# Kernel optimization log

Measured on AMD Instinct MI355X. Metric: run time of the kernel, lower is better.

Reference implementation:

```python
import jax, jax.numpy as jnp
import numpy as np
import math

EMBED_DIM = 1024
NUM_HEADS = 16
NUM_KV_HEADS = 16
DEPTH = 12
HEAD_DIM = EMBED_DIM // NUM_HEADS // 2  # 32
LAMBDA_INIT = 0.8 - 0.6 * math.exp(-0.3 * DEPTH)
EPS = 1e-5
THETA = 0.0001


def rope(q):
    # q: (b, s, h, d) with interleaved pairs, matches apply_rotary_pos_emb
    b, s, h, d = q.shape
    pos = jnp.arange(s, dtype=jnp.float32)[:, None]                      # (s,1)
    freq = 1.0 / (THETA ** (2.0 * jnp.arange(d // 2, dtype=jnp.float32) / d))
    ang = pos * freq                                                     # (s, d/2)
    cos = jnp.cos(ang)[None, :, None, :].astype(q.dtype)
    sin = jnp.sin(ang)[None, :, None, :].astype(q.dtype)
    qr = q.reshape(b, s, h, d // 2, 2)
    q0, q1 = qr[..., 0], qr[..., 1]
    out = jnp.stack([q0 * cos - q1 * sin, q0 * sin + q1 * cos], axis=-1)
    return out.reshape(q.shape)


def setup_inputs() -> dict:
    key = jax.random.key(0)
    ks = jax.random.split(key, 10)
    d = EMBED_DIM
    sd = 1.0 / math.sqrt(d)
    return {
        "x": jax.random.normal(ks[0], (1, 2048, d), dtype=jnp.float32),
        "Wq": jax.random.normal(ks[1], (d, d), dtype=jnp.float32) * sd,
        "Wk": jax.random.normal(ks[2], (d, d), dtype=jnp.float32) * sd,
        "Wv": jax.random.normal(ks[3], (d, d), dtype=jnp.float32) * sd,
        "Wo": jax.random.normal(ks[4], (d, d), dtype=jnp.float32) * sd,
        "lambda_q1": jax.random.normal(ks[5], (HEAD_DIM,), dtype=jnp.float32) * 0.1,
        "lambda_k1": jax.random.normal(ks[6], (HEAD_DIM,), dtype=jnp.float32) * 0.1,
        "lambda_q2": jax.random.normal(ks[7], (HEAD_DIM,), dtype=jnp.float32) * 0.1,
        "lambda_k2": jax.random.normal(ks[8], (HEAD_DIM,), dtype=jnp.float32) * 0.1,
        "subln_g": jnp.ones((2 * HEAD_DIM,), dtype=jnp.float32),
    }


def reference(x, Wq, Wk, Wv, Wo, lambda_q1, lambda_k1, lambda_q2, lambda_k2, subln_g):
    b, s, d = x.shape
    H, hd = NUM_HEADS, HEAD_DIM
    scaling = hd ** (-0.5)

    q = (x @ Wq).reshape(b, s, 2 * H, hd)
    k = (x @ Wk).reshape(b, s, 2 * NUM_KV_HEADS, hd)
    v = (x @ Wv).reshape(b, s, NUM_KV_HEADS, 2 * hd)

    q = rope(q).transpose(0, 2, 1, 3) * scaling   # (b, 2H, s, hd)
    k = rope(k).transpose(0, 2, 1, 3)             # (b, 2H, s, hd)  (n_rep = 1)
    v = v.transpose(0, 2, 1, 3)                   # (b, H, s, 2hd)

    scores = jnp.einsum("bhqd,bhkd->bhqk", q, k)  # (b, 2H, s, s)
    probs = jax.nn.softmax(scores.astype(jnp.float32), axis=-1).astype(scores.dtype)

    lam1 = jnp.exp(jnp.sum(lambda_q1 * lambda_k1))
    lam2 = jnp.exp(jnp.sum(lambda_q2 * lambda_k2))
    lam = (lam1 - lam2 + LAMBDA_INIT).astype(q.dtype)

    probs = probs.reshape(b, H, 2, s, s)
    w = probs[:, :, 0] - lam * probs[:, :, 1]     # (b, H, s, s)

    attn = jnp.einsum("bhqk,bhkd->bhqd", w, v)    # (b, H, s, 2hd)
    rms = jax.lax.rsqrt(jnp.mean(attn * attn, axis=-1, keepdims=True) + EPS)
    attn = attn * rms * subln_g
    attn = attn * (1.0 - LAMBDA_INIT)

    attn = attn.transpose(0, 2, 1, 3).reshape(b, s, H * 2 * hd)
    return attn @ Wo
```

## Files before the change

kernel.cpp:

```cpp
#include <hip/hip_runtime.h>
#include <math.h>

#define S 2048
#define D 1024
#define NH 16
#define HD 32
#define HD2 64

static constexpr float SCALE_Q_EXP2  = 0.17677669529663687f * 1.4426950408889634f;
static constexpr float LAMBDA_INIT_F = 0.78360576653162450f;
static constexpr float ONE_MINUS_LI  = 0.21639423346837553f;

typedef unsigned short u16;
typedef unsigned int   u32;
typedef __attribute__((ext_vector_type(4)))  unsigned short u16x4;
typedef __attribute__((ext_vector_type(8)))  short          bfrag;
typedef __attribute__((ext_vector_type(16))) float          f16acc;
typedef __attribute__((ext_vector_type(4)))  unsigned int   uint4v;

__device__ __forceinline__ u16 f2bf(float f) {
    u32 u = __builtin_bit_cast(u32, f);
    return (u16)((u + 0x7FFFu + ((u >> 16) & 1u)) >> 16);
}
__device__ __forceinline__ f16acc fillv(float v) {
    f16acc z;
#pragma unroll
    for (int i = 0; i < 16; ++i) z[i] = v;
    return z;
}
__device__ __forceinline__ float exp2_raw(float x) {
#if __has_builtin(__builtin_amdgcn_exp2f)
    return __builtin_amdgcn_exp2f(x);
#else
    float r;
    asm volatile("v_exp_f32 %0, %1\n\ts_nop 1" : "=v"(r) : "v"(x));
    return r;
#endif
}
#define MFMA(a, b, c) __builtin_amdgcn_mfma_f32_32x32x16_bf16(a, b, c, 0, 0, 0)

__device__ __forceinline__ void gload16(const u16* src, u16* lds) {
    __builtin_amdgcn_global_load_lds((const __attribute__((address_space(1))) void*)src,
                                     (__attribute__((address_space(3))) void*)lds, 16, 0, 0);
}

__global__ void prep_kernel(const float* __restrict__ lq1, const float* __restrict__ lk1,
                            const float* __restrict__ lq2, const float* __restrict__ lk2,
                            float* __restrict__ cosT, float* __restrict__ sinT,
                            float* __restrict__ lamOut) {
    int idx = blockIdx.x * blockDim.x + threadIdx.x;
    if (idx < S * 16) {
        int p = idx >> 4;
        int m = idx & 15;
        const double base = (double)1.0e-4f;
        float pf   = (float)pow(base, (double)m * (1.0 / 16.0));
        float freq = 1.0f / pf;
        float angf = (float)p * freq;
        double a = (double)angf;
        cosT[idx] = (float)cos(a);
        sinT[idx] = (float)sin(a);
    }
    if (blockIdx.x == 0 && threadIdx.x == 0) {
        float s1 = 0.f, s2 = 0.f;
        for (int i = 0; i < HD; ++i) {
            s1 += lq1[i] * lk1[i];
            s2 += lq2[i] * lk2[i];
        }
        *lamOut = expf(s1) - expf(s2) + LAMBDA_INIT_F;
    }
}

__global__ __launch_bounds__(256)
void convert_kernel(const float* __restrict__ x,  const float* __restrict__ Wq,
                    const float* __restrict__ Wk, const float* __restrict__ Wv,
                    const float* __restrict__ Wo,
                    u16* __restrict__ xb,  u16* __restrict__ WqT, u16* __restrict__ WkT,
                    u16* __restrict__ WvT, u16* __restrict__ WoT) {
    const int z = blockIdx.y;
    if (z == 0) {
        const int i = blockIdx.x * 256 + threadIdx.x;
        const float4 v = *(const float4*)&x[(size_t)i * 4];
        u16x4 r; r.x = f2bf(v.x); r.y = f2bf(v.y); r.z = f2bf(v.z); r.w = f2bf(v.w);
        *(u16x4*)&xb[(size_t)i * 4] = r;
        return;
    }
    const int b = blockIdx.x;
    if (b >= 256) return;
    __shared__ u16 Ts[64][66];
    const float* W = (z == 1) ? Wq : (z == 2) ? Wk : (z == 3) ? Wv : Wo;
    u16* T = (z == 1) ? WqT : (z == 2) ? WkT : (z == 3) ? WvT : WoT;
    const int k0 = (b >> 4) * 64, n0 = (b & 15) * 64;
    const int rg = threadIdx.x >> 4, cc = (threadIdx.x & 15) * 4;
#pragma unroll
    for (int i = 0; i < 4; ++i) {
        const int r = rg * 4 + i;
        const float4 v = *(const float4*)&W[(size_t)(k0 + r) * D + n0 + cc];
        Ts[r][cc + 0] = f2bf(v.x); Ts[r][cc + 1] = f2bf(v.y);
        Ts[r][cc + 2] = f2bf(v.z); Ts[r][cc + 3] = f2bf(v.w);
    }
    __syncthreads();
#pragma unroll
    for (int i = 0; i < 4; ++i) {
        const int rn = rg * 4 + i;
        u16x4 res;
        res.x = Ts[cc + 0][rn]; res.y = Ts[cc + 1][rn];
        res.z = Ts[cc + 2][rn]; res.w = Ts[cc + 3][rn];
        *(u16x4*)&T[(size_t)(n0 + rn) * D + k0 + cc] = res;
    }
}

template<int MODE>
__global__ __launch_bounds__(256)
void mm_kernel(const u16* __restrict__ Ab, const u16* __restrict__ B0,
               const u16* __restrict__ B1, const u16* __restrict__ B2,
               const float* __restrict__ cosT, const float* __restrict__ sinT,
               u16* __restrict__ Qb, u16* __restrict__ Kb2, u16* __restrict__ VT,
               float* __restrict__ Of) {
    __shared__ u16 As[128 * 32];
    __shared__ u16 Bs[128 * 32];

    const int nb   = blockIdx.x;
    const int row0 = blockIdx.y * 128;
    const int tid  = threadIdx.x;
    const int wave = tid >> 6;
    const int lane = tid & 63;
    const int ql   = lane & 31;
    const int hi   = lane >> 5;
    const int wr   = wave >> 1;
    const int wc   = wave & 1;

    const u16* Bt;
    int col0B;
    if (MODE == 0) {
        Bt = (nb < 8) ? B0 : (nb < 16) ? B1 : B2;
        col0B = (nb & 7) * 128;
    } else {
        Bt = B0;
        col0B = nb * 128;
    }

    const int rIn  = lane >> 2;
    const int kof  = 8 * (lane & 3);
    const size_t aRow0 = (size_t)(row0 + 16 * wave       + rIn) * D + kof;
    const size_t aRow1 = (size_t)(row0 + 16 * (wave + 4) + rIn) * D + kof;
    const size_t bRow0 = (size_t)(col0B + 16 * wave       + rIn) * D + kof;
    const size_t bRow1 = (size_t)(col0B + 16 * (wave + 4) + rIn) * D + kof;
    u16* ldsA0 = &As[512 * wave + 8 * lane];
    u16* ldsA1 = &As[512 * (wave + 4) + 8 * lane];
    u16* ldsB0 = &Bs[512 * wave + 8 * lane];
    u16* ldsB1 = &Bs[512 * (wave + 4) + 8 * lane];

    const int aoff = (wr * 64 + ql) * 32 + hi * 8;
    const int boff = (wc * 64 + ql) * 32 + hi * 8;

    f16acc acc00 = fillv(0.f), acc01 = fillv(0.f), acc10 = fillv(0.f), acc11 = fillv(0.f);

    for (int kk = 0; kk < D; kk += 32) {
        gload16(Ab + aRow0 + kk, ldsA0);
        gload16(Ab + aRow1 + kk, ldsA1);
        gload16(Bt + bRow0 + kk, ldsB0);
        gload16(Bt + bRow1 + kk, ldsB1);
        __syncthreads();
#pragma unroll
        for (int ks = 0; ks < 2; ++ks) {
            const bfrag a0 = *(const bfrag*)&As[aoff + ks * 16];
            const bfrag a1 = *(const bfrag*)&As[aoff + 32 * 32 + ks * 16];
            const bfrag b0 = *(const bfrag*)&Bs[boff + ks * 16];
            const bfrag b1 = *(const bfrag*)&Bs[boff + 32 * 32 + ks * 16];
            acc00 = MFMA(a0, b0, acc00);
            acc01 = MFMA(a0, b1, acc01);
            acc10 = MFMA(a1, b0, acc10);
            acc11 = MFMA(a1, b1, acc11);
        }
        __syncthreads();
    }

    f16acc accA[2][2];
    accA[0][0] = acc00; accA[0][1] = acc01; accA[1][0] = acc10; accA[1][1] = acc11;

    if (MODE == 0 && nb < 8) {
        const int m = ql >> 1;
        const bool ev = (ql & 1) == 0;
#pragma unroll
        for (int i = 0; i < 2; ++i)
#pragma unroll
        for (int j = 0; j < 2; ++j) {
            const int n = (nb & 7) * 128 + wc * 64 + j * 32 + ql;
            const int head = n >> 5;
            u16* hb = Qb + (size_t)head * S * HD;
#pragma unroll
            for (int r = 0; r < 16; ++r) {
                const int row = row0 + wr * 64 + i * 32 + 4 * hi + (r & 3) + 8 * (r >> 2);
                const float self = accA[i][j][r];
                const float part = __shfl_xor(self, 1);
                const float c = cosT[(row << 4) + m], s = sinT[(row << 4) + m];
                const float res = ev ? (self * c - part * s) : (part * s + self * c);
                hb[(size_t)row * HD + ql] = f2bf(res * SCALE_Q_EXP2);
            }
        }
    } else if (MODE == 0 && nb < 16) {
        const int m = ql >> 1;
        const bool ev = (ql & 1) == 0;
#pragma unroll
        for (int i = 0; i < 2; ++i)
#pragma unroll
        for (int j = 0; j < 2; ++j) {
            const int n = (nb & 7) * 128 + wc * 64 + j * 32 + ql;
            const int h2 = n >> 5;
            const int d  = n & 31;
            const int dpl = (d >> 3) * 256 + (d & 7);
            u16* hb = Kb2 + (size_t)h2 * 65536;
#pragma unroll
            for (int r = 0; r < 16; ++r) {
                const int row = row0 + wr * 64 + i * 32 + 4 * hi + (r & 3) + 8 * (r >> 2);
                const float self = accA[i][j][r];
                const float part = __shfl_xor(self, 1);
                const float c = cosT[(row << 4) + m], s = sinT[(row << 4) + m];
                const float res = ev ? (self * c - part * s) : (part * s + self * c);
                hb[(row >> 5) * 1024 + dpl + (row & 31) * 8] = f2bf(res);
            }
        }
    } else if (MODE == 0) {
#pragma unroll
        for (int i = 0; i < 2; ++i)
#pragma unroll
        for (int j = 0; j < 2; ++j) {
            const int n = (nb & 7) * 128 + wc * 64 + j * 32 + ql;
            const int head = n >> 6, d = n & 63;
            const int dt = d >> 5, dl = d & 31;
            u16* tb = VT + (size_t)head * 131072;
#pragma unroll
            for (int q = 0; q < 4; ++q) {
                const int row = row0 + wr * 64 + i * 32 + 4 * hi + 8 * q;
                const int idx = (row >> 5) * 2048 + (dt * 4 + q) * 256 + dl * 8 + 4 * hi;
                u16x4 res;
                res.x = f2bf(accA[i][j][4 * q + 0]);
                res.y = f2bf(accA[i][j][4 * q + 1]);
                res.z = f2bf(accA[i][j][4 * q + 2]);
                res.w = f2bf(accA[i][j][4 * q + 3]);
                *(u16x4*)&tb[idx] = res;
            }
        }
    } else {
#pragma unroll
        for (int i = 0; i < 2; ++i)
#pragma unroll
        for (int j = 0; j < 2; ++j) {
            const int gcol = col0B + wc * 64 + j * 32 + ql;
#pragma unroll
            for (int r = 0; r < 16; ++r) {
                const int row = row0 + wr * 64 + i * 32 + 4 * hi + (r & 3) + 8 * (r >> 2);
                Of[(size_t)row * D + gcol] = accA[i][j][r];
            }
        }
    }
}

__global__ __launch_bounds__(512, 2)
void attn_mfma(const u16* __restrict__ Qb, const u16* __restrict__ Kb2,
               const u16* __restrict__ Vt2, const float* __restrict__ lamPtr,
               const float* __restrict__ g, u16* __restrict__ AO) {
    const int bid  = blockIdx.x;
    const int h    = (bid & 7) * 2 + ((bid >> 3) >> 5);
    const int bx   = (bid >> 3) & 31;
    const int tid  = threadIdx.x;
    const int wave = tid >> 6;
    const int lane = tid & 63;
    const int hi   = lane >> 5;
    const int ql   = lane & 31;
    const int t    = wave >> 2;
    const int wv   = wave & 3;
    const int q0   = (bx * 2 + t) * 32;
    const int cbase = wv * 16;

    __shared__ float CMB[2][64][66];

    const u16* qp1 = Qb + ((size_t)(2 * h) * S + q0 + ql) * HD + 8 * hi;
    const u16* qp2 = qp1 + (size_t)S * HD;
    bfrag qf1[2], qf2[2];
    qf1[0] = *(const bfrag*)(qp1);      qf1[1] = *(const bfrag*)(qp1 + 16);
    qf2[0] = *(const bfrag*)(qp2);      qf2[1] = *(const bfrag*)(qp2 + 16);

    const u16* k1g = Kb2 + (size_t)(2 * h) * 65536;
    const u16* k2g = k1g + 65536;
    const u16* vg  = Vt2 + (size_t)h * 131072;
    const int kro  = ql * 8;

    const f16acc ZR = fillv(0.f);
    uint4v ou; ou[0] = ou[1] = ou[2] = ou[3] = 0x3F803F80u;
    const bfrag ONES = __builtin_bit_cast(bfrag, ou);

    f16acc acc1[2], acc2[2];
    acc1[0] = fillv(0.f); acc1[1] = fillv(0.f);
    acc2[0] = fillv(0.f); acc2[1] = fillv(0.f);
    float l1 = 0.f, l2 = 0.f;

    bfrag kA1[2], kA2[2], kB1[2], kB2[2];
    bfrag vA[2][2], vB[2][2];
#pragma unroll
    for (int s = 0; s < 2; ++s) {
        kA1[s] = *(const bfrag*)(k1g + (size_t)cbase * 1024 + (2 * s + hi) * 256 + kro);
        kA2[s] = *(const bfrag*)(k2g + (size_t)cbase * 1024 + (2 * s + hi) * 256 + kro);
#pragma unroll
        for (int dt = 0; dt < 2; ++dt)
            vA[s][dt] = *(const bfrag*)(vg + (size_t)cbase * 2048 + (dt * 4 + 2 * s + hi) * 256 + kro);
    }

    auto body = [&](bfrag (&kc1)[2], bfrag (&kc2)[2], bfrag (&vc)[2][2],
                    bfrag (&kn1)[2], bfrag (&kn2)[2], bfrag (&vn)[2][2], int cn) {
        const u16* k1c = k1g + (size_t)cn * 1024;
        const u16* k2c = k2g + (size_t)cn * 1024;
        const u16* vvc = vg + (size_t)cn * 2048;
#pragma unroll
        for (int s = 0; s < 2; ++s) {
            kn1[s] = *(const bfrag*)(k1c + (2 * s + hi) * 256 + kro);
            kn2[s] = *(const bfrag*)(k2c + (2 * s + hi) * 256 + kro);
#pragma unroll
            for (int dt = 0; dt < 2; ++dt)
                vn[s][dt] = *(const bfrag*)(vvc + (dt * 4 + 2 * s + hi) * 256 + kro);
        }

        __builtin_amdgcn_s_setprio(1);
        f16acc s1 = MFMA(kc1[0], qf1[0], ZR);  s1 = MFMA(kc1[1], qf1[1], s1);
        f16acc s2 = MFMA(kc2[0], qf2[0], ZR);  s2 = MFMA(kc2[1], qf2[1], s2);
        __builtin_amdgcn_s_setprio(0);

#pragma unroll
        for (int r = 0; r < 16; ++r) {
            s1[r] = exp2_raw(s1[r]);
            s2[r] = exp2_raw(s2[r]);
        }

        u32 w1[8], w2[8];
#pragma unroll
        for (int j = 0; j < 8; ++j) {
            asm("v_cvt_pk_bf16_f32 %0, %1, %2" : "=v"(w1[j]) : "v"(s1[2 * j]), "v"(s1[2 * j + 1]));
            asm("v_cvt_pk_bf16_f32 %0, %1, %2" : "=v"(w2[j]) : "v"(s2[2 * j]), "v"(s2[2 * j + 1]));
        }
        asm("v_permlane32_swap_b32 %0, %1" : "+v"(w1[0]), "+v"(w1[2]));
        asm("v_permlane32_swap_b32 %0, %1" : "+v"(w1[1]), "+v"(w1[3]));
        asm("v_permlane32_swap_b32 %0, %1" : "+v"(w1[4]), "+v"(w1[6]));
        asm("v_permlane32_swap_b32 %0, %1" : "+v"(w1[5]), "+v"(w1[7]));
        asm("v_permlane32_swap_b32 %0, %1" : "+v"(w2[0]), "+v"(w2[2]));
        asm("v_permlane32_swap_b32 %0, %1" : "+v"(w2[1]), "+v"(w2[3]));
        asm("v_permlane32_swap_b32 %0, %1" : "+v"(w2[4]), "+v"(w2[6]));
        asm("v_permlane32_swap_b32 %0, %1" : "+v"(w2[5]), "+v"(w2[7]));
        uint4v u;
        bfrag p1[2], p2[2];
        u[0] = w1[0]; u[1] = w1[1]; u[2] = w1[2]; u[3] = w1[3];
        p1[0] = __builtin_bit_cast(bfrag, u);
        u[0] = w1[4]; u[1] = w1[5]; u[2] = w1[6]; u[3] = w1[7];
        p1[1] = __builtin_bit_cast(bfrag, u);
        u[0] = w2[0]; u[1] = w2[1]; u[2] = w2[2]; u[3] = w2[3];
        p2[0] = __builtin_bit_cast(bfrag, u);
        u[0] = w2[4]; u[1] = w2[5]; u[2] = w2[6]; u[3] = w2[7];
        p2[1] = __builtin_bit_cast(bfrag, u);

        __builtin_amdgcn_s_setprio(1);
        acc1[0] = MFMA(vc[0][0], p1[0], acc1[0]);
        acc1[0] = MFMA(vc[1][0], p1[1], acc1[0]);
        acc1[1] = MFMA(vc[0][1], p1[0], acc1[1]);
        acc1[1] = MFMA(vc[1][1], p1[1], acc1[1]);
        acc2[0] = MFMA(vc[0][0], p2[0], acc2[0]);
        acc2[0] = MFMA(vc[1][0], p2[1], acc2[0]);
        acc2[1] = MFMA(vc[0][1], p2[0], acc2[1]);
        acc2[1] = MFMA(vc[1][1], p2[1], acc2[1]);
        f16acc t1 = MFMA(ONES, p1[0], ZR);  t1 = MFMA(ONES, p1[1], t1);
        f16acc t2 = MFMA(ONES, p2[0], ZR);  t2 = MFMA(ONES, p2[1], t2);
        __builtin_amdgcn_s_setprio(0);
        l1 += t1[0];
        l2 += t2[0];
    };

    for (int i = 0; i < 16; i += 2) {
        const int c0 = cbase + i;
        body(kA1, kA2, vA, kB1, kB2, vB, c0 + 1);
        const int c2 = (i + 2 < 16) ? c0 + 2 : c0 + 1;
        body(kB1, kB2, vB, kA1, kA2, vA, c2);
    }

#pragma unroll 1
    for (int p = 1; p < 4; ++p) {
        if (wv == p) {
            float* c0 = &CMB[t][lane][0];
#pragma unroll
            for (int dt = 0; dt < 2; ++dt)
#pragma unroll
                for (int r = 0; r < 16; ++r) {
                    c0[dt * 16 + r]      = acc1[dt][r];
                    c0[32 + dt * 16 + r] = acc2[dt][r];
                }
            c0[64] = l1; c0[65] = l2;
        }
        __syncthreads();
        if (wv == 0) {
            const float* c0 = &CMB[t][lane][0];
#pragma unroll
            for (int dt = 0; dt < 2; ++dt)
#pragma unroll
                for (int r = 0; r < 16; ++r) {
                    acc1[dt][r] += c0[dt * 16 + r];
                    acc2[dt][r] += c0[32 + dt * 16 + r];
                }
            l1 += c0[64]; l2 += c0[65];
        }
        __syncthreads();
    }

    if (wv == 0) {
        const float lam = *lamPtr;
        const float inv1 = 1.0f / l1, inv2 = 1.0f / l2;
        float o_[2][16];
        float ss = 0.f;
#pragma unroll
        for (int dt = 0; dt < 2; ++dt)
#pragma unroll
            for (int r = 0; r < 16; ++r) {
                float o = acc1[dt][r] * inv1 - lam * (acc2[dt][r] * inv2);
                o_[dt][r] = o;
                ss += o * o;
            }
        ss += __shfl_xor(ss, 32);
        const float rs = rsqrtf(ss * (1.0f / 64.0f) + 1e-5f);

        u16* aorow = AO + (size_t)(q0 + ql) * D + h * 64;
#pragma unroll
        for (int dt = 0; dt < 2; ++dt)
#pragma unroll
            for (int G = 0; G < 4; ++G) {
                const int dbase = dt * 32 + G * 8 + hi * 4;
                const float4 gv = *(const float4*)&g[dbase];
                u16x4 res;
                res.x = f2bf(o_[dt][4 * G + 0] * rs * gv.x * ONE_MINUS_LI);
                res.y = f2bf(o_[dt][4 * G + 1] * rs * gv.y * ONE_MINUS_LI);
                res.z = f2bf(o_[dt][4 * G + 2] * rs * gv.z * ONE_MINUS_LI);
                res.w = f2bf(o_[dt][4 * G + 3] * rs * gv.w * ONE_MINUS_LI);
                *(u16x4*)&aorow[dbase] = res;
            }
    }
}

extern "C" void kernel_launch(void* const* d_in, const int* in_sizes, int n_in,
                              void* d_out, int out_size, void* d_ws, size_t ws_size,
                              hipStream_t stream) {
    const float* x   = (const float*)d_in[0];
    const float* Wq  = (const float*)d_in[1];
    const float* Wk  = (const float*)d_in[2];
    const float* Wv  = (const float*)d_in[3];
    const float* Wo  = (const float*)d_in[4];
    const float* lq1 = (const float*)d_in[5];
    const float* lk1 = (const float*)d_in[6];
    const float* lq2 = (const float*)d_in[7];
    const float* lk2 = (const float*)d_in[8];
    const float* g   = (const float*)d_in[9];
    float* out = (float*)d_out;

    char* ws = (char*)d_ws;
    float* cosT = (float*)(ws);
    float* sinT = (float*)(ws + 131072);
    float* lam  = (float*)(ws + 262144);
    char*  b    = ws + 262400;
    u16*   Qb   = (u16*)(b);
    u16*   Kb2  = (u16*)(b + 4194304);
    u16*   VT   = (u16*)(b + 8388608);
    u16*   AO   = (u16*)(b + 12582912);
    u16*   xb   = (u16*)(b + 16777216);
    u16*   WqT  = (u16*)(b + 20971520);
    u16*   WkT  = (u16*)(b + 23068672);
    u16*   WvT  = (u16*)(b + 25165824);
    u16*   WoT  = (u16*)(b + 27262976);

    prep_kernel<<<128, 256, 0, stream>>>(lq1, lk1, lq2, lk2, cosT, sinT, lam);
    convert_kernel<<<dim3(2048, 5), 256, 0, stream>>>(x, Wq, Wk, Wv, Wo,
                                                      xb, WqT, WkT, WvT, WoT);

    mm_kernel<0><<<dim3(24, 16), 256, 0, stream>>>(xb, WqT, WkT, WvT, cosT, sinT,
                                                   Qb, Kb2, VT, nullptr);

    attn_mfma<<<512, 512, 0, stream>>>(Qb, Kb2, VT, lam, g, AO);

    mm_kernel<1><<<dim3(8, 16), 256, 0, stream>>>(AO, WoT, nullptr, nullptr, cosT, sinT,
                                                  nullptr, nullptr, nullptr, out);
}
```

Baseline: 107.7 us.

## Software-pipeline attention loop so PV MFMA of previous chunk overlaps softmax

New measurement: 114.3 us. 6.2% more time.

```diff
diff --git a/kernel.cpp b/kernel.cpp
--- a/kernel.cpp
+++ b/kernel.cpp
@@ -295,42 +295,33 @@
     acc2[0] = fillv(0.f); acc2[1] = fillv(0.f);
     float l1 = 0.f, l2 = 0.f;
 
-    bfrag kA1[2], kA2[2], kB1[2], kB2[2];
-    bfrag vA[2][2], vB[2][2];
-#pragma unroll
-    for (int s = 0; s < 2; ++s) {
-        kA1[s] = *(const bfrag*)(k1g + (size_t)cbase * 1024 + (2 * s + hi) * 256 + kro);
-        kA2[s] = *(const bfrag*)(k2g + (size_t)cbase * 1024 + (2 * s + hi) * 256 + kro);
-#pragma unroll
-        for (int dt = 0; dt < 2; ++dt)
-            vA[s][dt] = *(const bfrag*)(vg + (size_t)cbase * 2048 + (dt * 4 + 2 * s + hi) * 256 + kro);
-    }
-
-    auto body = [&](bfrag (&kc1)[2], bfrag (&kc2)[2], bfrag (&vc)[2][2],
-                    bfrag (&kn1)[2], bfrag (&kn2)[2], bfrag (&vn)[2][2], int cn) {
-        const u16* k1c = k1g + (size_t)cn * 1024;
-        const u16* k2c = k2g + (size_t)cn * 1024;
-        const u16* vvc = vg + (size_t)cn * 2048;
+    bfrag K1s[2][2], K2s[2][2];
+    bfrag Vs[3][2][2];
+    bfrag pC1[2], pC2[2];
+
+    auto loadK = [&](int set, int c) {
+        const u16* k1c = k1g + (size_t)c * 1024;
+        const u16* k2c = k2g + (size_t)c * 1024;
 #pragma unroll
         for (int s = 0; s < 2; ++s) {
-            kn1[s] = *(const bfrag*)(k1c + (2 * s + hi) * 256 + kro);
-            kn2[s] = *(const bfrag*)(k2c + (2 * s + hi) * 256 + kro);
+            K1s[set][s] = *(const bfrag*)(k1c + (2 * s + hi) * 256 + kro);
+            K2s[set][s] = *(const bfrag*)(k2c + (2 * s + hi) * 256 + kro);
+        }
+    };
+    auto loadV = [&](int set, int c) {
+        const u16* vvc = vg + (size_t)c * 2048;
+#pragma unroll
+        for (int s = 0; s < 2; ++s)
 #pragma unroll
             for (int dt = 0; dt < 2; ++dt)
-                vn[s][dt] = *(const bfrag*)(vvc + (dt * 4 + 2 * s + hi) * 256 + kro);
-        }
-
-        __builtin_amdgcn_s_setprio(1);
-        f16acc s1 = MFMA(kc1[0], qf1[0], ZR);  s1 = MFMA(kc1[1], qf1[1], s1);
-        f16acc s2 = MFMA(kc2[0], qf2[0], ZR);  s2 = MFMA(kc2[1], qf2[1], s2);
-        __builtin_amdgcn_s_setprio(0);
-
+                Vs[set][s][dt] = *(const bfrag*)(vvc + (dt * 4 + 2 * s + hi) * 256 + kro);
+    };
+    auto doSM = [&](f16acc& s1, f16acc& s2) {
 #pragma unroll
         for (int r = 0; r < 16; ++r) {
             s1[r] = exp2_raw(s1[r]);
             s2[r] = exp2_raw(s2[r]);
         }
-
         u32 w1[8], w2[8];
 #pragma unroll
         for (int j = 0; j < 8; ++j) {
@@ -346,38 +337,60 @@
         asm("v_permlane32_swap_b32 %0, %1" : "+v"(w2[4]), "+v"(w2[6]));
         asm("v_permlane32_swap_b32 %0, %1" : "+v"(w2[5]), "+v"(w2[7]));
         uint4v u;
-        bfrag p1[2], p2[2];
         u[0] = w1[0]; u[1] = w1[1]; u[2] = w1[2]; u[3] = w1[3];
-        p1[0] = __builtin_bit_cast(bfrag, u);
+        pC1[0] = __builtin_bit_cast(bfrag, u);
         u[0] = w1[4]; u[1] = w1[5]; u[2] = w1[6]; u[3] = w1[7];
-        p1[1] = __builtin_bit_cast(bfrag, u);
+        pC1[1] = __builtin_bit_cast(bfrag, u);
         u[0] = w2[0]; u[1] = w2[1]; u[2] = w2[2]; u[3] = w2[3];
-        p2[0] = __builtin_bit_cast(bfrag, u);
+        pC2[0] = __builtin_bit_cast(bfrag, u);
         u[0] = w2[4]; u[1] = w2[5]; u[2] = w2[6]; u[3] = w2[7];
-        p2[1] = __builtin_bit_cast(bfrag, u);
-
+        pC2[1] = __builtin_bit_cast(bfrag, u);
+    };
+    auto doPV = [&](int vset) {
         __builtin_amdgcn_s_setprio(1);
-        acc1[0] = MFMA(vc[0][0], p1[0], acc1[0]);
-        acc1[0] = MFMA(vc[1][0], p1[1], acc1[0]);
-        acc1[1] = MFMA(vc[0][1], p1[0], acc1[1]);
-        acc1[1] = MFMA(vc[1][1], p1[1], acc1[1]);
-        acc2[0] = MFMA(vc[0][0], p2[0], acc2[0]);
-        acc2[0] = MFMA(vc[1][0], p2[1], acc2[0]);
-        acc2[1] = MFMA(vc[0][1], p2[0], acc2[1]);
-        acc2[1] = MFMA(vc[1][1], p2[1], acc2[1]);
-        f16acc t1 = MFMA(ONES, p1[0], ZR);  t1 = MFMA(ONES, p1[1], t1);
-        f16acc t2 = MFMA(ONES, p2[0], ZR);  t2 = MFMA(ONES, p2[1], t2);
+        acc1[0] = MFMA(Vs[vset][0][0], pC1[0], acc1[0]);
+        acc1[0] = MFMA(Vs[vset][1][0], pC1[1], acc1[0]);
+        acc1[1] = MFMA(Vs[vset][0][1], pC1[0], acc1[1]);
+        acc1[1] = MFMA(Vs[vset][1][1], pC1[1], acc1[1]);
+        acc2[0] = MFMA(Vs[vset][0][0], pC2[0], acc2[0]);
+        acc2[0] = MFMA(Vs[vset][1][0], pC2[1], acc2[0]);
+        acc2[1] = MFMA(Vs[vset][0][1], pC2[0], acc2[1]);
+        acc2[1] = MFMA(Vs[vset][1][1], pC2[1], acc2[1]);
+        f16acc t1 = MFMA(ONES, pC1[0], ZR);  t1 = MFMA(ONES, pC1[1], t1);
+        f16acc t2 = MFMA(ONES, pC2[0], ZR);  t2 = MFMA(ONES, pC2[1], t2);
         __builtin_amdgcn_s_setprio(0);
         l1 += t1[0];
         l2 += t2[0];
     };
 
-    for (int i = 0; i < 16; i += 2) {
-        const int c0 = cbase + i;
-        body(kA1, kA2, vA, kB1, kB2, vB, c0 + 1);
-        const int c2 = (i + 2 < 16) ? c0 + 2 : c0 + 1;
-        body(kB1, kB2, vB, kA1, kA2, vA, c2);
-    }
+    loadK(0, cbase);  loadV(0, cbase);
+    loadK(1, cbase + 1);  loadV(1, cbase + 1);
+    {
+        __builtin_amdgcn_s_setprio(1);
+        f16acc s1 = MFMA(K1s[0][0], qf1[0], ZR);  s1 = MFMA(K1s[0][1], qf1[1], s1);
+        f16acc s2 = MFMA(K2s[0][0], qf2[0], ZR);  s2 = MFMA(K2s[0][1], qf2[1], s2);
+        __builtin_amdgcn_s_setprio(0);
+        doSM(s1, s2);
+    }
+
+#pragma unroll
+    for (int j = 1; j <= 15; ++j) {
+        const int cs = j & 1;
+        const int ns = (j + 1) & 1;
+        const int vp = (j - 1) % 3;
+        const int vn = (j + 1) % 3;
+        const int cn = (j < 15) ? cbase + j + 1 : cbase + 15;
+        loadK(ns, cn);  loadV(vn, cn);
+
+        __builtin_amdgcn_s_setprio(1);
+        f16acc s1 = MFMA(K1s[cs][0], qf1[0], ZR);  s1 = MFMA(K1s[cs][1], qf1[1], s1);
+        f16acc s2 = MFMA(K2s[cs][0], qf2[0], ZR);  s2 = MFMA(K2s[cs][1], qf2[1], s2);
+        __builtin_amdgcn_s_setprio(0);
+
+        doPV(vp);
+        doSM(s1, s2);
+    }
+    doPV(15 % 3);
 
 #pragma unroll 1
     for (int p = 1; p < 4; ++p) {
```
